# Kernel tuning notes

Hardware: AMD Instinct MI355X
Metric: run time of the kernel (lower is better)

The kernel has to match this reference:

```python
import jax, jax.numpy as jnp
import numpy as np

N_NODES = 100000
N_EDGES = 3200000
IN_DIM = 128
OUT_DIM = 64
ITERS = 2


def setup_inputs() -> dict:
    key = jax.random.key(0)
    k1, k2, k3, k4, k5, k6 = jax.random.split(key, 6)
    feature = jax.random.normal(k1, (N_NODES, IN_DIM), dtype=jnp.float32)
    src = jax.random.randint(k2, (N_EDGES,), 0, N_NODES, dtype=jnp.int32)
    dst = jax.random.randint(k3, (N_EDGES,), 0, N_NODES, dtype=jnp.int32)
    # Kaiming-ish scaling for stability
    W_lin = jax.random.normal(k4, (IN_DIM, OUT_DIM), dtype=jnp.float32) / np.sqrt(IN_DIM)
    W_d1 = jax.random.normal(k5, (OUT_DIM, OUT_DIM), dtype=jnp.float32) / np.sqrt(OUT_DIM)
    W_d2 = jax.random.normal(k6, (OUT_DIM, OUT_DIM), dtype=jnp.float32) / np.sqrt(OUT_DIM)
    return {"feature": feature, "src": src, "dst": dst,
            "W_lin": W_lin, "W_d1": W_d1, "W_d2": W_d2}


def reference(feature, src, dst, W_lin, W_d1, W_d2):
    # u_i^0 = 0 ; u_i^j = tanh(linear(x_i) + dense(sum_{k in N(i)} u_k^{j-1}))
    base = feature @ W_lin                       # [N, OUT_DIM] (no bias)
    n = feature.shape[0]
    u = jnp.zeros((n, OUT_DIM), dtype=feature.dtype)
    for _ in range(ITERS):
        # copy_u + sum: message u[src] scattered-summed at dst
        m = jax.ops.segment_sum(u[src], dst, num_segments=n)   # [N, OUT_DIM]
        # Dense (2 layers, relu between, no bias): W_d2 @ relu(W_d1 @ m)
        h = jax.nn.relu(m @ W_d1) @ W_d2
        u = jnp.tanh(base + h)
    return u
```

## Files before the change

### kernel.cpp

```cpp
#include <hip/hip_runtime.h>
#include <math.h>

#define N_NODES 100000
#define N_EDGES 3200000
#define IN_DIM  128
#define OUT_DIM 64

#define BSHIFT   7
#define BNODES   128
#define NBUCKETS ((N_NODES + BNODES - 1) / BNODES)
#define NBINBLK  1024
#define CHUNK    (N_EDGES / NBINBLK)
#define SEGCAP   6144
#define MTILES   (N_NODES / 16)

typedef _Float16 half8 __attribute__((ext_vector_type(8)));
typedef float    f32x4 __attribute__((ext_vector_type(4)));

__device__ __forceinline__ float rl(float v, int l) {
    return __int_as_float(__builtin_amdgcn_readlane(__float_as_int(v), l));
}

__device__ __forceinline__ int xcd_swz(int i) {
    return (i & 7) * (NBINBLK / 8) + (i >> 3);
}

__global__ __launch_bounds__(256) void gemm_base_tanh(
    const float* __restrict__ feature,
    const float* __restrict__ Wlin,
    float* __restrict__ base,
    _Float16* __restrict__ u1h)
{
    int lane = threadIdx.x & 63;
    int wid  = (blockIdx.x * 256 + threadIdx.x) >> 6;
    if (wid >= MTILES) return;

    int mrow = lane & 15;
    int kb   = lane >> 4;
    int k0   = kb * 8;

    half8 b[4][4];
#pragma unroll
    for (int s = 0; s < 4; ++s)
#pragma unroll
        for (int n = 0; n < 4; ++n)
#pragma unroll
            for (int j = 0; j < 8; ++j)
                b[s][n][j] = (_Float16)Wlin[(s * 32 + k0 + j) * OUT_DIM + n * 16 + mrow];

    int row = wid * 16 + mrow;
    const float4* fr = reinterpret_cast<const float4*>(feature + (size_t)row * IN_DIM);
    half8 a[4];
#pragma unroll
    for (int s = 0; s < 4; ++s) {
        float4 lo = fr[(s * 32 + k0) >> 2];
        float4 hi = fr[((s * 32 + k0) >> 2) + 1];
        a[s][0] = (_Float16)lo.x; a[s][1] = (_Float16)lo.y;
        a[s][2] = (_Float16)lo.z; a[s][3] = (_Float16)lo.w;
        a[s][4] = (_Float16)hi.x; a[s][5] = (_Float16)hi.y;
        a[s][6] = (_Float16)hi.z; a[s][7] = (_Float16)hi.w;
    }

    f32x4 acc[4];
#pragma unroll
    for (int n = 0; n < 4; ++n) acc[n] = (f32x4)0.f;

#pragma unroll
    for (int s = 0; s < 4; ++s)
#pragma unroll
        for (int n = 0; n < 4; ++n)
            acc[n] = __builtin_amdgcn_mfma_f32_16x16x32_f16(a[s], b[s][n], acc[n], 0, 0, 0);

#pragma unroll
    for (int n = 0; n < 4; ++n)
#pragma unroll
        for (int j = 0; j < 4; ++j) {
            int r = wid * 16 + kb * 4 + j;
            int c = n * 16 + mrow;
            float v = acc[n][j];
            base[(size_t)r * OUT_DIM + c] = v;
            u1h[(size_t)r * OUT_DIM + c] = (_Float16)tanhf(v);
        }
}

__global__ __launch_bounds__(256) void bin_hist(
    const int* __restrict__ dst, int* __restrict__ H)
{
    __shared__ int h[NBUCKETS];
    for (int k = threadIdx.x; k < NBUCKETS; k += 256) h[k] = 0;
    __syncthreads();

    int b = xcd_swz(blockIdx.x);
    int beg = b * CHUNK, end = beg + CHUNK;
    for (int i = beg + threadIdx.x; i < end; i += 256)
        atomicAdd(&h[dst[i] >> BSHIFT], 1);
    __syncthreads();

    for (int k = threadIdx.x; k < NBUCKETS; k += 256)
        H[(size_t)k * NBINBLK + b] = h[k];
}

__global__ __launch_bounds__(NBINBLK) void scan_local(
    int* __restrict__ H, int* __restrict__ Btot)
{
    __shared__ int s[NBINBLK];
    int k = blockIdx.x, t = threadIdx.x;
    int v = H[(size_t)k * NBINBLK + t];
    s[t] = v;
    __syncthreads();
#pragma unroll
    for (int off = 1; off < NBINBLK; off <<= 1) {
        int x = (t >= off) ? s[t - off] : 0;
        __syncthreads();
        s[t] += x;
        __syncthreads();
    }
    H[(size_t)k * NBINBLK + t] = s[t] - v;
    if (t == NBINBLK - 1) Btot[k] = s[t];
}

__global__ __launch_bounds__(1024) void scan_tot(int* __restrict__ Btot)
{
    __shared__ int s[1024];
    int t = threadIdx.x;
    int v = (t < NBUCKETS) ? Btot[t] : 0;
    s[t] = v;
    __syncthreads();
#pragma unroll
    for (int off = 1; off < 1024; off <<= 1) {
        int x = (t >= off) ? s[t - off] : 0;
        __syncthreads();
        s[t] += x;
        __syncthreads();
    }
    if (t < NBUCKETS) Btot[t] = s[t] - v;
}

__global__ __launch_bounds__(NBINBLK) void add_base(
    int* __restrict__ H, const int* __restrict__ Btot)
{
    int k = blockIdx.x, t = threadIdx.x;
    H[(size_t)k * NBINBLK + t] += Btot[k];
    if (k == 0 && t == 0) H[(size_t)NBUCKETS * NBINBLK] = N_EDGES;
}

__global__ __launch_bounds__(256) void bin_scatter(
    const int* __restrict__ src,
    const int* __restrict__ dst,
    const int* __restrict__ H,
    int* __restrict__ ebuf)
{
    __shared__ int cur[NBUCKETS];
    int b = xcd_swz(blockIdx.x);
    for (int k = threadIdx.x; k < NBUCKETS; k += 256)
        cur[k] = H[(size_t)k * NBINBLK + b];
    __syncthreads();

    int beg = b * CHUNK, end = beg + CHUNK;
    for (int i = beg + threadIdx.x; i < end; i += 256) {
        int d = dst[i];
        int k = d >> BSHIFT;
        int p = atomicAdd(&cur[k], 1);
        ebuf[p] = src[i] | ((d & (BNODES - 1)) << 17);
    }
}

__global__ __launch_bounds__(256) void bucket_sort(
    const int* __restrict__ H,
    int* __restrict__ ebuf,
    int* __restrict__ node_off)
{
    __shared__ int seg[SEGCAP];
    __shared__ int cnt[BNODES];
    __shared__ int off[BNODES];
    int k = blockIdx.x;
    int beg = H[(size_t)k * NBINBLK];
    int end = H[(size_t)(k + 1) * NBINBLK];
    int n = end - beg;

    for (int j = threadIdx.x; j < BNODES; j += 256) cnt[j] = 0;
    __syncthreads();

    for (int i = threadIdx.x; i < n; i += 256) {
        int v = ebuf[beg + i];
        seg[i] = v;
        atomicAdd(&cnt[v >> 17], 1);
    }
    __syncthreads();

    if (threadIdx.x == 0) {
        int node0 = k * BNODES;
        int nvalid = N_NODES - node0; if (nvalid > BNODES) nvalid = BNODES;
        int excl = 0;
        for (int j = 0; j < nvalid; ++j) {
            off[j] = excl;
            node_off[node0 + j] = beg + excl;
            excl += cnt[j];
        }
        if (k == NBUCKETS - 1) node_off[N_NODES] = end;
    }
    __syncthreads();

    for (int i = threadIdx.x; i < n; i += 256) {
        int v = seg[i];
        int p = atomicAdd(&off[v >> 17], 1);
        ebuf[beg + p] = v & 0x1FFFF;
    }
}

__global__ __launch_bounds__(256) void node_gather(
    const int* __restrict__ node_off,
    const int* __restrict__ csr,
    const half8* __restrict__ u1v,
    float* __restrict__ m)
{
    int wid = (blockIdx.x * 256 + threadIdx.x) >> 6;
    if (wid >= N_NODES) return;
    int lane = threadIdx.x & 63;
    int q = lane >> 3, c = lane & 7;

    int beg = node_off[wid];
    int end = node_off[wid + 1];

    float acc[8];
#pragma unroll
    for (int i = 0; i < 8; ++i) acc[i] = 0.f;

    int e = beg + q;
    for (; e + 24 < end; e += 32) {
        int s0 = csr[e];
        int s1 = csr[e + 8];
        int s2 = csr[e + 16];
        int s3 = csr[e + 24];
        half8 a = u1v[(size_t)s0 * 8 + c];
        half8 b = u1v[(size_t)s1 * 8 + c];
        half8 g = u1v[(size_t)s2 * 8 + c];
        half8 d = u1v[(size_t)s3 * 8 + c];
#pragma unroll
        for (int i = 0; i < 8; ++i)
            acc[i] += ((float)a[i] + (float)b[i]) + ((float)g[i] + (float)d[i]);
    }
    for (; e < end; e += 8) {
        half8 a = u1v[(size_t)csr[e] * 8 + c];
#pragma unroll
        for (int i = 0; i < 8; ++i) acc[i] += (float)a[i];
    }

#pragma unroll
    for (int i = 0; i < 8; ++i) {
        acc[i] += __shfl_xor(acc[i], 8);
        acc[i] += __shfl_xor(acc[i], 16);
        acc[i] += __shfl_xor(acc[i], 32);
    }

    if (q == 0) {
        float4* mr = reinterpret_cast<float4*>(m + (size_t)wid * OUT_DIM + c * 8);
        mr[0] = make_float4(acc[0], acc[1], acc[2], acc[3]);
        mr[1] = make_float4(acc[4], acc[5], acc[6], acc[7]);
    }
}

__global__ __launch_bounds__(256) void dense_tanh(
    const float* __restrict__ m,
    const float* __restrict__ W1,
    const float* __restrict__ W2,
    const float* __restrict__ base,
    float* __restrict__ out)
{
    __shared__ _Float16 tl[4][16][72];
    int lane = threadIdx.x & 63;
    int w    = threadIdx.x >> 6;
    int wid  = (blockIdx.x * 256 + threadIdx.x) >> 6;
    if (wid >= MTILES) return;

    int mrow = lane & 15;
    int kb   = lane >> 4;
    int k0   = kb * 8;

    half8 b1[2][4], b2[2][4];
#pragma unroll
    for (int s = 0; s < 2; ++s)
#pragma unroll
        for (int n = 0; n < 4; ++n)
#pragma unroll
            for (int j = 0; j < 8; ++j) {
                b1[s][n][j] = (_Float16)W1[(s * 32 + k0 + j) * 64 + n * 16 + mrow];
                b2[s][n][j] = (_Float16)W2[(s * 32 + k0 + j) * 64 + n * 16 + mrow];
            }

    int row = wid * 16 + mrow;
    const float4* mr = reinterpret_cast<const float4*>(m + (size_t)row * 64);
    half8 a[2];
#pragma unroll
    for (int s = 0; s < 2; ++s) {
        float4 lo = mr[(s * 32 + k0) >> 2];
        float4 hi = mr[((s * 32 + k0) >> 2) + 1];
        a[s][0] = (_Float16)lo.x; a[s][1] = (_Float16)lo.y;
        a[s][2] = (_Float16)lo.z; a[s][3] = (_Float16)lo.w;
        a[s][4] = (_Float16)hi.x; a[s][5] = (_Float16)hi.y;
        a[s][6] = (_Float16)hi.z; a[s][7] = (_Float16)hi.w;
    }

    f32x4 acc1[4];
#pragma unroll
    for (int n = 0; n < 4; ++n) acc1[n] = (f32x4)0.f;
#pragma unroll
    for (int s = 0; s < 2; ++s)
#pragma unroll
        for (int n = 0; n < 4; ++n)
            acc1[n] = __builtin_amdgcn_mfma_f32_16x16x32_f16(a[s], b1[s][n], acc1[n], 0, 0, 0);

#pragma unroll
    for (int n = 0; n < 4; ++n)
#pragma unroll
        for (int j = 0; j < 4; ++j)
            tl[w][kb * 4 + j][n * 16 + mrow] = (_Float16)fmaxf(acc1[n][j], 0.f);

    half8 a2[2];
#pragma unroll
    for (int s = 0; s < 2; ++s)
        a2[s] = *reinterpret_cast<const half8*>(&tl[w][mrow][s * 32 + k0]);

    f32x4 acc2[4];
#pragma unroll
    for (int n = 0; n < 4; ++n) acc2[n] = (f32x4)0.f;
#pragma unroll
    for (int s = 0; s < 2; ++s)
#pragma unroll
        for (int n = 0; n < 4; ++n)
            acc2[n] = __builtin_amdgcn_mfma_f32_16x16x32_f16(a2[s], b2[s][n], acc2[n], 0, 0, 0);

#pragma unroll
    for (int n = 0; n < 4; ++n)
#pragma unroll
        for (int j = 0; j < 4; ++j) {
            int r = wid * 16 + kb * 4 + j;
            int c = n * 16 + mrow;
            out[(size_t)r * 64 + c] = tanhf(base[(size_t)r * 64 + c] + acc2[n][j]);
        }
}

extern "C" void kernel_launch(void* const* d_in, const int* in_sizes, int n_in,
                              void* d_out, int out_size, void* d_ws, size_t ws_size,
                              hipStream_t stream)
{
    const float* feature = (const float*)d_in[0];
    const int*   src     = (const int*)d_in[1];
    const int*   dst     = (const int*)d_in[2];
    const float* W_lin   = (const float*)d_in[3];
    const float* W_d1    = (const float*)d_in[4];
    const float* W_d2    = (const float*)d_in[5];
    float* out = (float*)d_out;

    const size_t NODE_F = (size_t)N_NODES * OUT_DIM;

    float*    base     = (float*)d_ws;
    _Float16* u1h      = (_Float16*)(base + NODE_F);
    float*    m        = (float*)(u1h + NODE_F);
    int*      H        = (int*)(m + NODE_F);
    int*      Btot     = H + ((size_t)NBUCKETS * NBINBLK + 4);
    int*      node_off = Btot + (NBUCKETS + 4);
    int*      ebuf     = node_off + (N_NODES + 4);

    int gemm_blocks = (MTILES + 3) / 4;
    gemm_base_tanh<<<gemm_blocks, 256, 0, stream>>>(feature, W_lin, base, u1h);

    bin_hist  <<<NBINBLK, 256, 0, stream>>>(dst, H);
    scan_local<<<NBUCKETS, NBINBLK, 0, stream>>>(H, Btot);
    scan_tot  <<<1, 1024, 0, stream>>>(Btot);
    add_base  <<<NBUCKETS, NBINBLK, 0, stream>>>(H, Btot);
    bin_scatter<<<NBINBLK, 256, 0, stream>>>(src, dst, H, ebuf);
    bucket_sort<<<NBUCKETS, 256, 0, stream>>>(H, ebuf, node_off);

    int gather_blocks = (int)(((size_t)N_NODES * 64 + 255) / 256);
    node_gather<<<gather_blocks, 256, 0, stream>>>(
        node_off, ebuf, (const half8*)u1h, m);

    dense_tanh<<<gemm_blocks, 256, 0, stream>>>(m, W_d1, W_d2, base, out);
}
```

Baseline: 168.3 us.

## Store base in fp16, fuse bucket totals into histogram, contiguous per-lane gather ranges

The base projection is stored as fp16 instead of fp32, halving its write and read traffic. Bucket totals are accumulated atomically in the histogram kernel, so the scan pipeline drops the add_base kernel and runs the total scan before the local scan, which now adds the offset itself. In node_gather, each 8-lane group takes a contiguous slice of the neighbor list rather than a strided one, so index loads are sequential. The fp16 base adds rounding error to the output, and the memset plus global atomics add a little overhead.

```diff
diff --git a/kernel.cpp b/kernel.cpp
--- a/kernel.cpp
+++ b/kernel.cpp
@@ -17,10 +17,6 @@
 typedef _Float16 half8 __attribute__((ext_vector_type(8)));
 typedef float    f32x4 __attribute__((ext_vector_type(4)));
 
-__device__ __forceinline__ float rl(float v, int l) {
-    return __int_as_float(__builtin_amdgcn_readlane(__float_as_int(v), l));
-}
-
 __device__ __forceinline__ int xcd_swz(int i) {
     return (i & 7) * (NBINBLK / 8) + (i >> 3);
 }
@@ -28,7 +24,7 @@
 __global__ __launch_bounds__(256) void gemm_base_tanh(
     const float* __restrict__ feature,
     const float* __restrict__ Wlin,
-    float* __restrict__ base,
+    _Float16* __restrict__ baseh,
     _Float16* __restrict__ u1h)
 {
     int lane = threadIdx.x & 63;
@@ -78,13 +74,13 @@
             int r = wid * 16 + kb * 4 + j;
             int c = n * 16 + mrow;
             float v = acc[n][j];
-            base[(size_t)r * OUT_DIM + c] = v;
-            u1h[(size_t)r * OUT_DIM + c] = (_Float16)tanhf(v);
+            baseh[(size_t)r * OUT_DIM + c] = (_Float16)v;
+            u1h[(size_t)r * OUT_DIM + c]  = (_Float16)tanhf(v);
         }
 }
 
 __global__ __launch_bounds__(256) void bin_hist(
-    const int* __restrict__ dst, int* __restrict__ H)
+    const int* __restrict__ dst, int* __restrict__ H, int* __restrict__ tot)
 {
     __shared__ int h[NBUCKETS];
     for (int k = threadIdx.x; k < NBUCKETS; k += 256) h[k] = 0;
@@ -96,12 +92,34 @@
         atomicAdd(&h[dst[i] >> BSHIFT], 1);
     __syncthreads();
 
-    for (int k = threadIdx.x; k < NBUCKETS; k += 256)
-        H[(size_t)k * NBINBLK + b] = h[k];
+    for (int k = threadIdx.x; k < NBUCKETS; k += 256) {
+        int v = h[k];
+        H[(size_t)k * NBINBLK + b] = v;
+        if (v) atomicAdd(&tot[k], v);
+    }
+}
+
+__global__ __launch_bounds__(1024) void scan_tot(
+    int* __restrict__ Btot, int* __restrict__ H)
+{
+    __shared__ int s[1024];
+    int t = threadIdx.x;
+    int v = (t < NBUCKETS) ? Btot[t] : 0;
+    s[t] = v;
+    __syncthreads();
+#pragma unroll
+    for (int off = 1; off < 1024; off <<= 1) {
+        int x = (t >= off) ? s[t - off] : 0;
+        __syncthreads();
+        s[t] += x;
+        __syncthreads();
+    }
+    if (t < NBUCKETS) Btot[t] = s[t] - v;
+    if (t == 0) H[(size_t)NBUCKETS * NBINBLK] = N_EDGES;
 }
 
 __global__ __launch_bounds__(NBINBLK) void scan_local(
-    int* __restrict__ H, int* __restrict__ Btot)
+    int* __restrict__ H, const int* __restrict__ Btot)
 {
     __shared__ int s[NBINBLK];
     int k = blockIdx.x, t = threadIdx.x;
@@ -115,33 +133,7 @@
         s[t] += x;
         __syncthreads();
     }
-    H[(size_t)k * NBINBLK + t] = s[t] - v;
-    if (t == NBINBLK - 1) Btot[k] = s[t];
-}
-
-__global__ __launch_bounds__(1024) void scan_tot(int* __restrict__ Btot)
-{
-    __shared__ int s[1024];
-    int t = threadIdx.x;
-    int v = (t < NBUCKETS) ? Btot[t] : 0;
-    s[t] = v;
-    __syncthreads();
-#pragma unroll
-    for (int off = 1; off < 1024; off <<= 1) {
-        int x = (t >= off) ? s[t - off] : 0;
-        __syncthreads();
-        s[t] += x;
-        __syncthreads();
-    }
-    if (t < NBUCKETS) Btot[t] = s[t] - v;
-}
-
-__global__ __launch_bounds__(NBINBLK) void add_base(
-    int* __restrict__ H, const int* __restrict__ Btot)
-{
-    int k = blockIdx.x, t = threadIdx.x;
-    H[(size_t)k * NBINBLK + t] += Btot[k];
-    if (k == 0 && t == 0) H[(size_t)NBUCKETS * NBINBLK] = N_EDGES;
+    H[(size_t)k * NBINBLK + t] = (s[t] - v) + Btot[k];
 }
 
 __global__ __launch_bounds__(256) void bin_scatter(
@@ -221,17 +213,21 @@
 
     int beg = node_off[wid];
     int end = node_off[wid + 1];
+    int cnt = end - beg;
+    int per = (cnt + 7) >> 3;
+    int gb  = beg + q * per;
+    int ge  = gb + per; if (ge > end) ge = end;
 
     float acc[8];
 #pragma unroll
     for (int i = 0; i < 8; ++i) acc[i] = 0.f;
 
-    int e = beg + q;
-    for (; e + 24 < end; e += 32) {
+    int e = gb;
+    for (; e + 4 <= ge; e += 4) {
         int s0 = csr[e];
-        int s1 = csr[e + 8];
-        int s2 = csr[e + 16];
-        int s3 = csr[e + 24];
+        int s1 = csr[e + 1];
+        int s2 = csr[e + 2];
+        int s3 = csr[e + 3];
         half8 a = u1v[(size_t)s0 * 8 + c];
         half8 b = u1v[(size_t)s1 * 8 + c];
         half8 g = u1v[(size_t)s2 * 8 + c];
@@ -240,7 +236,7 @@
         for (int i = 0; i < 8; ++i)
             acc[i] += ((float)a[i] + (float)b[i]) + ((float)g[i] + (float)d[i]);
     }
-    for (; e < end; e += 8) {
+    for (; e < ge; ++e) {
         half8 a = u1v[(size_t)csr[e] * 8 + c];
 #pragma unroll
         for (int i = 0; i < 8; ++i) acc[i] += (float)a[i];
@@ -264,7 +260,7 @@
     const float* __restrict__ m,
     const float* __restrict__ W1,
     const float* __restrict__ W2,
-    const float* __restrict__ base,
+    const _Float16* __restrict__ baseh,
     float* __restrict__ out)
 {
     __shared__ _Float16 tl[4][16][72];
@@ -336,7 +332,8 @@
         for (int j = 0; j < 4; ++j) {
             int r = wid * 16 + kb * 4 + j;
             int c = n * 16 + mrow;
-            out[(size_t)r * 64 + c] = tanhf(base[(size_t)r * 64 + c] + acc2[n][j]);
+            float b0 = (float)baseh[(size_t)r * 64 + c];
+            out[(size_t)r * 64 + c] = tanhf(b0 + acc2[n][j]);
         }
 }
 
@@ -354,21 +351,22 @@
 
     const size_t NODE_F = (size_t)N_NODES * OUT_DIM;
 
-    float*    base     = (float*)d_ws;
-    _Float16* u1h      = (_Float16*)(base + NODE_F);
+    _Float16* baseh    = (_Float16*)d_ws;
+    _Float16* u1h      = baseh + NODE_F;
     float*    m        = (float*)(u1h + NODE_F);
     int*      H        = (int*)(m + NODE_F);
-    int*      Btot     = H + ((size_t)NBUCKETS * NBINBLK + 4);
-    int*      node_off = Btot + (NBUCKETS + 4);
+    int*      tot      = H + ((size_t)NBUCKETS * NBINBLK + 4);
+    int*      node_off = tot + (NBUCKETS + 4);
     int*      ebuf     = node_off + (N_NODES + 4);
 
+    hipMemsetAsync(tot, 0, NBUCKETS * sizeof(int), stream);
+
     int gemm_blocks = (MTILES + 3) / 4;
-    gemm_base_tanh<<<gemm_blocks, 256, 0, stream>>>(feature, W_lin, base, u1h);
-
-    bin_hist  <<<NBINBLK, 256, 0, stream>>>(dst, H);
-    scan_local<<<NBUCKETS, NBINBLK, 0, stream>>>(H, Btot);
-    scan_tot  <<<1, 1024, 0, stream>>>(Btot);
-    add_base  <<<NBUCKETS, NBINBLK, 0, stream>>>(H, Btot);
+    gemm_base_tanh<<<gemm_blocks, 256, 0, stream>>>(feature, W_lin, baseh, u1h);
+
+    bin_hist  <<<NBINBLK, 256, 0, stream>>>(dst, H, tot);
+    scan_tot  <<<1, 1024, 0, stream>>>(tot, H);
+    scan_local<<<NBUCKETS, NBINBLK, 0, stream>>>(H, tot);
     bin_scatter<<<NBINBLK, 256, 0, stream>>>(src, dst, H, ebuf);
     bucket_sort<<<NBUCKETS, 256, 0, stream>>>(H, ebuf, node_off);
 
@@ -376,5 +374,5 @@
     node_gather<<<gather_blocks, 256, 0, stream>>>(
         node_off, ebuf, (const half8*)u1h, m);
 
-    dense_tanh<<<gemm_blocks, 256, 0, stream>>>(m, W_d1, W_d2, base, out);
-}
+    dense_tanh<<<gemm_blocks, 256, 0, stream>>>(m, W_d1, W_d2, baseh, out);
+}
```

Measured after the change: 200.2 us. 19.0% more time.
